# Kernel optimization log

Hardware: AMD Instinct MI355X
Metric: run time of the kernel (lower is better)

Reference implementation:

```python
import jax, jax.numpy as jnp
import numpy as np

B = 128
N0, N1, N2, N3 = 3072, 1536, 768, 384
DEG = 16
NUM_FEAT = 3
DIM_CELL = 8
ND = 32
ED = 64
IN_DRUG = 77
DIM_DRUG = 128
BN_EPS = 1e-5


def _pool_edges(e, cluster):
    # PyG max_pool edge pooling: relabel endpoints by cluster, drop self-loops, coalesce
    ce = cluster[e]
    ce = ce[:, ce[0] != ce[1]]
    return np.unique(ce, axis=1)


def setup_inputs():
    rng = np.random.default_rng(0)
    e0 = np.stack([rng.integers(0, N0, N0 * DEG), rng.integers(0, N0, N0 * DEG)])
    c0 = np.arange(N0) // 2
    c1 = np.arange(N1) // 2
    c2 = np.arange(N2) // 2
    e1 = _pool_edges(e0, c0)
    e2 = _pool_edges(e1, c1)
    de = np.stack([rng.integers(0, ND, ED), rng.integers(0, ND, ED)])
    be = lambda e, n: np.concatenate([e + j * n for j in range(B)], axis=1)
    bc = lambda c, k: np.concatenate([c + j * k for j in range(B)])
    keys = iter(jax.random.split(jax.random.key(0), 64))

    def lin(fi, fo):
        s = 1.0 / float(np.sqrt(fi))
        return (jax.random.uniform(next(keys), (fi, fo), jnp.float32, -s, s),
                jax.random.uniform(next(keys), (fo,), jnp.float32, -s, s))

    inp = {}
    inp["cell_x"] = jax.random.normal(next(keys), (B * N0, NUM_FEAT), jnp.float32)
    inp["drug_x"] = jax.random.normal(next(keys), (B * ND, IN_DRUG), jnp.float32)
    inp["cell_edges0"] = jnp.asarray(be(e0, N0), jnp.int32)
    inp["cell_edges1"] = jnp.asarray(be(e1, N1), jnp.int32)
    inp["cell_edges2"] = jnp.asarray(be(e2, N2), jnp.int32)
    inp["cluster0"] = jnp.asarray(bc(c0, N1), jnp.int32)
    inp["cluster1"] = jnp.asarray(bc(c1, N2), jnp.int32)
    inp["cluster2"] = jnp.asarray(bc(c2, N3), jnp.int32)
    inp["drug_edges"] = jnp.asarray(be(de, ND), jnp.int32)
    inp["drug_batch"] = jnp.asarray(np.repeat(np.arange(B), ND), jnp.int32)
    for i, fi in enumerate([NUM_FEAT, DIM_CELL, DIM_CELL]):
        W, b = lin(fi, DIM_CELL)
        inp[f"gat_W{i}"] = W
        inp[f"gat_b{i}"] = b
        inp[f"gat_as{i}"] = 0.1 * jax.random.normal(next(keys), (DIM_CELL,), jnp.float32)
        inp[f"gat_ad{i}"] = 0.1 * jax.random.normal(next(keys), (DIM_CELL,), jnp.float32)
    for i, fi in enumerate([IN_DRUG, DIM_DRUG, DIM_DRUG]):
        W1, b1 = lin(fi, DIM_DRUG)
        W2, b2 = lin(DIM_DRUG, DIM_DRUG)
        inp[f"gin_W1_{i}"] = W1
        inp[f"gin_b1_{i}"] = b1
        inp[f"gin_W2_{i}"] = W2
        inp[f"gin_b2_{i}"] = b2
        inp[f"bn_w{i}"] = jnp.ones((DIM_DRUG,), jnp.float32)
        inp[f"bn_b{i}"] = jnp.zeros((DIM_DRUG,), jnp.float32)
    inp["demb_W"], inp["demb_b"] = lin(3 * DIM_DRUG, 256)
    inp["cemb_W1"], inp["cemb_b1"] = lin(N3 * DIM_CELL, 1024)
    inp["cemb_W2"], inp["cemb_b2"] = lin(1024, 256)
    inp["reg_W1"], inp["reg_b1"] = lin(512, 512)
    inp["reg_W2"], inp["reg_b2"] = lin(512, 512)
    inp["reg_W3"], inp["reg_b3"] = lin(512, 1)
    return inp


def _bn(x, w=None, b=None):
    # training-mode BatchNorm1d (biased variance over the node dim)
    xn = (x - x.mean(0)) / jnp.sqrt(x.var(0) + BN_EPS)
    return xn if w is None else xn * w + b


def _gat(x, edges, W, a_s, a_d, b, n):
    # single-head GATConv with self-loops, negative_slope=0.2
    h = x @ W  # [n, d]
    loop = jnp.arange(n, dtype=edges.dtype)
    src = jnp.concatenate([edges[0], loop])
    dst = jnp.concatenate([edges[1], loop])
    logit = jax.nn.leaky_relu((h @ a_s)[src] + (h @ a_d)[dst], 0.2)
    m = jax.ops.segment_max(logit, dst, num_segments=n)
    e = jnp.exp(logit - m[dst])
    s = jax.ops.segment_sum(e, dst, num_segments=n)
    alpha = e / s[dst]
    return jax.ops.segment_sum(alpha[:, None] * h[src], dst, num_segments=n) + b


def _forward(floats, ints):
    (cell_x, drug_x,
     gat_W0, gat_b0, gat_as0, gat_ad0,
     gat_W1, gat_b1, gat_as1, gat_ad1,
     gat_W2, gat_b2, gat_as2, gat_ad2,
     gin_W1_0, gin_b1_0, gin_W2_0, gin_b2_0, bn_w0, bn_b0,
     gin_W1_1, gin_b1_1, gin_W2_1, gin_b2_1, bn_w1, bn_b1,
     gin_W1_2, gin_b1_2, gin_W2_2, gin_b2_2, bn_w2, bn_b2,
     demb_W, demb_b, cemb_W1, cemb_b1, cemb_W2, cemb_b2,
     reg_W1, reg_b1, reg_W2, reg_b2, reg_W3, reg_b3) = floats
    (cell_edges0, cell_edges1, cell_edges2,
     cluster0, cluster1, cluster2, drug_edges, drug_batch) = ints

    nd = drug_x.shape[0]
    x = drug_x
    feats = []
    for W1, b1, W2, b2, bw, bb in [
            (gin_W1_0, gin_b1_0, gin_W2_0, gin_b2_0, bn_w0, bn_b0),
            (gin_W1_1, gin_b1_1, gin_W2_1, gin_b2_1, bn_w1, bn_b1),
            (gin_W1_2, gin_b1_2, gin_W2_2, gin_b2_2, bn_w2, bn_b2)]:
        agg = x + jax.ops.segment_sum(x[drug_edges[0]], drug_edges[1], num_segments=nd)
        x = jax.nn.relu(jax.nn.relu(agg @ W1 + b1) @ W2 + b2)
        x = _bn(x, bw, bb)
        feats.append(x)
    xd = jax.ops.segment_max(jnp.concatenate(feats, axis=1), drug_batch, num_segments=B)
    xd = jax.nn.relu(xd @ demb_W + demb_b)  # [B, 256]

    xc = cell_x
    layers = [(cell_edges0, cluster0, B * N0, B * N1, gat_W0, gat_as0, gat_ad0, gat_b0),
              (cell_edges1, cluster1, B * N1, B * N2, gat_W1, gat_as1, gat_ad1, gat_b1),
              (cell_edges2, cluster2, B * N2, B * N3, gat_W2, gat_as2, gat_ad2, gat_b2)]
    for e, cl, n_in, n_out, W, a_s, a_d, b in layers:
        xc = jax.nn.relu(_gat(xc, e, W, a_s, a_d, b, n_in))
        xc = jax.ops.segment_max(xc, cl, num_segments=n_out)
        xc = _bn(xc)
    xc = xc.reshape(B, N3 * DIM_CELL)  # [B, 3072]
    xc = jax.nn.relu(xc @ cemb_W1 + cemb_b1)
    xc = jax.nn.relu(xc @ cemb_W2 + cemb_b2)  # [B, 256]

    z = jnp.concatenate([xd, xc], axis=-1)  # [B, 512]
    z = jax.nn.elu(z @ reg_W1 + reg_b1)
    z = jax.nn.elu(z @ reg_W2 + reg_b2)
    return z @ reg_W3 + reg_b3  # [B, 1]


def reference(cell_x, drug_x, cell_edges0, cell_edges1, cell_edges2, cluster0, cluster1, cluster2,
              drug_edges, drug_batch,
              gat_W0, gat_b0, gat_as0, gat_ad0, gat_W1, gat_b1, gat_as1, gat_ad1,
              gat_W2, gat_b2, gat_as2, gat_ad2,
              gin_W1_0, gin_b1_0, gin_W2_0, gin_b2_0, bn_w0, bn_b0,
              gin_W1_1, gin_b1_1, gin_W2_1, gin_b2_1, bn_w1, bn_b1,
              gin_W1_2, gin_b1_2, gin_W2_2, gin_b2_2, bn_w2, bn_b2,
              demb_W, demb_b, cemb_W1, cemb_b1, cemb_W2, cemb_b2,
              reg_W1, reg_b1, reg_W2, reg_b2, reg_W3, reg_b3):
    floats = (cell_x, drug_x,
              gat_W0, gat_b0, gat_as0, gat_ad0, gat_W1, gat_b1, gat_as1, gat_ad1,
              gat_W2, gat_b2, gat_as2, gat_ad2,
              gin_W1_0, gin_b1_0, gin_W2_0, gin_b2_0, bn_w0, bn_b0,
              gin_W1_1, gin_b1_1, gin_W2_1, gin_b2_1, bn_w1, bn_b1,
              gin_W1_2, gin_b1_2, gin_W2_2, gin_b2_2, bn_w2, bn_b2,
              demb_W, demb_b, cemb_W1, cemb_b1, cemb_W2, cemb_b2,
              reg_W1, reg_b1, reg_W2, reg_b2, reg_W3, reg_b3)
    ints = (cell_edges0, cell_edges1, cell_edges2, cluster0, cluster1, cluster2, drug_edges, drug_batch)
    return _forward(floats, ints)
```

## Files before the change

kernel.cpp:

```cpp
#include <hip/hip_runtime.h>
#include <math.h>

#define CDIV(a,b) (((a)+(b)-1)/(b))


template<int ACT>
__launch_bounds__(256)
__global__ void gemm_kernel(const float* __restrict__ A, const float* __restrict__ W,
                            const float* __restrict__ bias, float* __restrict__ C,
                            int M, int N, int K, int ldc) {
    const int BM = 64, BN = 64, BK = 16;
    __shared__ float As[BK][BM];
    __shared__ float Ws[BK][BN];
    int tid = threadIdx.x;
    int brow = blockIdx.y * BM;
    int bcol = blockIdx.x * BN;
    int tr = (tid / 16) * 4;
    int tc = (tid % 16) * 4;
    float acc[4][4] = {};
    for (int k0 = 0; k0 < K; k0 += BK) {
        for (int i = tid; i < BM * BK; i += 256) {
            int r = i / BK, c = i % BK;
            int gr = brow + r, gc = k0 + c;
            As[c][r] = (gr < M && gc < K) ? A[(size_t)gr * K + gc] : 0.f;
// ... 23 lines not shown
        int gr = brow + tr + i;
        if (gr >= M) continue;
        #pragma unroll
        for (int j = 0; j < 4; ++j) {
            int gc = bcol + tc + j;
            if (gc >= N) continue;
            float v = acc[i][j] + bias[gc];
            if (ACT == 1) v = fmaxf(v, 0.f);
            if (ACT == 2) v = (v > 0.f) ? v : expm1f(v);
            C[(size_t)gr * ldc + gc] = v;
        }
    }
}

__launch_bounds__(256)
__global__ void gemm_part_kernel(const float* __restrict__ A, const float* __restrict__ W,
                                 float* __restrict__ Cp, int M, int N, int K, int KC) {
    const int BM = 64, BN = 64, BK = 16;
    __shared__ float As[BK][BM];
    __shared__ float Ws[BK][BN];
    int tid = threadIdx.x;
    int brow = blockIdx.y * BM;
    int bcol = blockIdx.x * BN;
    int s = blockIdx.z;
    int kb = s * KC, ke = min(K, kb + KC);
    int tr = (tid / 16) * 4;
    int tc = (tid % 16) * 4;
    float acc[4][4] = {};
    for (int k0 = kb; k0 < ke; k0 += BK) {
        for (int i = tid; i < BM * BK; i += 256) {
// ... 48 lines not shown
}

__global__ void reg3_kernel(const float* __restrict__ z2, const float* __restrict__ W,
                            const float* __restrict__ b, float* __restrict__ out) {
    int gid = blockIdx.x * blockDim.x + threadIdx.x;
    int r = gid / 64;
    int lane = gid & 63;
    if (r >= 128) return;
    float a = 0.f;
    for (int c = lane; c < 512; c += 64) a += z2[(size_t)r * 512 + c] * W[c];
    #pragma unroll
    for (int o = 32; o > 0; o >>= 1) a += __shfl_down(a, o);
    if (lane == 0) out[r] = a + b[0];
}

__launch_bounds__(256)
__global__ void drug_agg_kernel(const int* __restrict__ edges, int E,
                                const float* __restrict__ x, float* __restrict__ agg, int F) {
    int g = blockIdx.x;
    __shared__ int es[64], ed[64];
    int t = threadIdx.x;
    if (t < 64) { es[t] = edges[g * 64 + t]; ed[t] = edges[E + g * 64 + t]; }
    __syncthreads();
    int base = g * 32;
    for (int idx = t; idx < 32 * F; idx += 256) {
        int node = idx / F, f = idx - node * F;
        int gn = base + node;
        float acc = x[(size_t)gn * F + f];
        #pragma unroll 4
        for (int e = 0; e < 64; ++e)
            if (ed[e] == gn) acc += x[(size_t)es[e] * F + f];
        agg[(size_t)gn * F + f] = acc;
    }
}

__global__ void drug_pool_kernel(const float* __restrict__ feats, float* __restrict__ xd) {
    int i = blockIdx.x * blockDim.x + threadIdx.x;
    if (i >= 128 * 384) return;
    int b = i / 384, f = i - b * 384;
    float m = -INFINITY;
    for (int r = 0; r < 32; ++r) m = fmaxf(m, feats[(size_t)(b * 32 + r) * 384 + f]);
    xd[i] = m;
}

__launch_bounds__(256)
__global__ void bn_stats_kernel(const float* __restrict__ x, int M, int N, float* __restrict__ sums) {
    int c = blockIdx.x;
    float s = 0.f, q = 0.f;
    for (int r = blockIdx.y * 256 + threadIdx.x; r < M; r += gridDim.y * 256) {
        float v = x[(size_t)r * N + c];
        s += v; q += v * v;
    }
    __shared__ float ss[256], qq[256];
    ss[threadIdx.x] = s; qq[threadIdx.x] = q;
    __syncthreads();
    for (int o = 128; o > 0; o >>= 1) {
        if (threadIdx.x < o) { ss[threadIdx.x] += ss[threadIdx.x + o]; qq[threadIdx.x] += qq[threadIdx.x + o]; }
        __syncthreads();
    }
    if (threadIdx.x == 0) { atomicAdd(&sums[c], ss[0]); atomicAdd(&sums[N + c], qq[0]); }
}

template<bool AFFINE>
__global__ void bn_apply_kernel(const float* __restrict__ x, const float* __restrict__ sums,
                                const float* __restrict__ w, const float* __restrict__ b,
                                float* __restrict__ out, float* __restrict__ out2,
                                int M, int N, int ldo2) {
    int i = blockIdx.x * blockDim.x + threadIdx.x;
    if (i >= M * N) return;
    int r = i / N, c = i - (i / N) * N;
    float mean = sums[c] / (float)M;
    float var  = sums[N + c] / (float)M - mean * mean;
    float inv  = rsqrtf(var + 1e-5f);
    float xn = (x[i] - mean) * inv;
    if (AFFINE) xn = xn * w[c] + b[c];
    out[i] = xn;
    if (out2) out2[(size_t)r * ldo2 + c] = xn;
}

template<bool BN>
__launch_bounds__(256)
__global__ void gat_proj_kernel(const float* __restrict__ x, const float* __restrict__ bnsums,
                                float minv, const float* __restrict__ W,
                                const float* __restrict__ a_s, const float* __restrict__ a_d,
                                float* __restrict__ h, float* __restrict__ hs, float* __restrict__ hd,
                                int n, int F) {
    __shared__ float smean[8], sinv[8];
    if (BN) {
        if (threadIdx.x < 8) {
            float mean = bnsums[threadIdx.x] * minv;
            float var  = bnsums[8 + threadIdx.x] * minv - mean * mean;
            smean[threadIdx.x] = mean;
            sinv[threadIdx.x]  = rsqrtf(var + 1e-5f);
        }
        __syncthreads();
    }
    int i = blockIdx.x * blockDim.x + threadIdx.x;
    if (i >= n) return;
    float acc[8];
    #pragma unroll
    for (int k = 0; k < 8; ++k) acc[k] = 0.f;
    for (int f = 0; f < F; ++f) {
        float xv = x[(size_t)i * F + f];
        if (BN) xv = (xv - smean[f]) * sinv[f];
        #pragma unroll
        for (int k = 0; k < 8; ++k) acc[k] += xv * W[f * 8 + k];
    }
    float s_ = 0.f, d_ = 0.f;
    #pragma unroll
    for (int k = 0; k < 8; ++k) {
        s_ += acc[k] * a_s[k];
        d_ += acc[k] * a_d[k];
    }
    float4* h4 = (float4*)(h + (size_t)i * 8);
    h4[0] = make_float4(acc[0], acc[1], acc[2], acc[3]);
    h4[1] = make_float4(acc[4], acc[5], acc[6], acc[7]);
    hs[i] = s_;
    hd[i] = d_;
}

__global__ void csr_count_kernel(const int* __restrict__ edges, int Eg, int Etot,
                                 int* __restrict__ deg) {
    int i = blockIdx.x * blockDim.x + threadIdx.x;
    if (i < Eg) atomicAdd(&deg[edges[Etot + i]], 1);
}

__launch_bounds__(256)
__global__ void scan_local_kernel(const int* __restrict__ deg, int* __restrict__ rowptr,
                                  int* __restrict__ bsum, int n) {
    __shared__ int sh[256];
    int base = blockIdx.x * 1024;
    int t = threadIdx.x;
    int v[4]; int s = 0;
    #pragma unroll
    for (int j = 0; j < 4; ++j) {
        int idx = base + t * 4 + j;
        v[j] = (idx < n) ? deg[idx] : 0;
        s += v[j];
    }
    sh[t] = s;
    __syncthreads();
    for (int o = 1; o < 256; o <<= 1) {
        int add = (t >= o) ? sh[t - o] : 0;
        __syncthreads();
        sh[t] += add;
        __syncthreads();
    }
    int excl = sh[t] - s;
    #pragma unroll
    for (int j = 0; j < 4; ++j) {
        int idx = base + t * 4 + j;
        if (idx < n) rowptr[idx] = excl;
        excl += v[j];
    }
    if (t == 255) bsum[blockIdx.x] = sh[255];
}

__launch_bounds__(256)
__global__ void scan_add_kernel(int* __restrict__ rowptr, const int* __restrict__ bsum, int n) {
    int b = blockIdx.x;
    int t = threadIdx.x;
    int acc = 0;
    for (int i = t; i < b; i += 256) acc += bsum[i];
    __shared__ int sh[256];
    sh[t] = acc;
    __syncthreads();
    for (int o = 128; o > 0; o >>= 1) {
        if (t < o) sh[t] += sh[t + o];
        __syncthreads();
    }
    int off = sh[0];
    int base = b * 1024;
    #pragma unroll
    for (int j = 0; j < 4; ++j) {
        int idx = base + t * 4 + j;
        if (idx < n) rowptr[idx] += off;
    }
}

__global__ void csr_fill_kernel(const int* __restrict__ edges, int Eg, int Etot,
                                const int* __restrict__ rowptr, int* __restrict__ cnt,
                                int* __restrict__ srclist) {
    int i = blockIdx.x * blockDim.x + threadIdx.x;
    if (i >= Eg) return;
    int s = edges[i], d = edges[Etot + i];
    int pos = rowptr[d] + atomicAdd(&cnt[d], 1);
    srclist[pos] = s;
}

__launch_bounds__(256)
__global__ void gat_gather_kernel(const int* __restrict__ rowptr, const int* __restrict__ deg,
                                  const int* __restrict__ srcl,
                                  const float* __restrict__ hs, const float* __restrict__ hd,
                                  const float* __restrict__ h, const float* __restrict__ bvec,
                                  float* __restrict__ pooled, float* __restrict__ sums,
                                  int n, int Nin, int Nout) {
    const int lane = threadIdx.x & 63;
    float4 bA = ((const float4*)bvec)[0];
    float4 bB = ((const float4*)bvec)[1];
    float ps[8] = {}, pq[8] = {};
    const float4* __restrict__ h4 = (const float4*)h;
    for (unsigned d = blockIdx.x * 256 + threadIdx.x; d < (unsigned)n; d += gridDim.x * 256) {
        unsigned b = d / (unsigned)Nin;
        unsigned dl = d - b * Nin;
        int base = b * Nin;
        float hdd = hd[d];
        float l = hs[d] + hdd;
        l = (l > 0.f) ? l : 0.2f * l;
        float e = __expf(l);
        float den = e;
        float4 sa = h4[2 * (size_t)d], sb = h4[2 * (size_t)d + 1];
        float n0 = e * sa.x, n1 = e * sa.y, n2 = e * sa.z, n3 = e * sa.w;
        float n4 = e * sb.x, n5 = e * sb.y, n6 = e * sb.z, n7 = e * sb.w;
        int j = rowptr[dl];
        int jend = j + deg[dl];
        for (; j + 2 <= jend; j += 2) {
            int s0 = srcl[j] + base;
            int s1 = srcl[j + 1] + base;
            float l0 = hs[s0] + hdd, l1 = hs[s1] + hdd;
            float4 a0 = h4[2 * (size_t)s0], b0 = h4[2 * (size_t)s0 + 1];
            float4 a1 = h4[2 * (size_t)s1], b1 = h4[2 * (size_t)s1 + 1];
            l0 = (l0 > 0.f) ? l0 : 0.2f * l0;
            l1 = (l1 > 0.f) ? l1 : 0.2f * l1;
            float e0 = __expf(l0), e1 = __expf(l1);
            den += e0 + e1;
            n0 += e0 * a0.x + e1 * a1.x;  n1 += e0 * a0.y + e1 * a1.y;
            n2 += e0 * a0.z + e1 * a1.z;  n3 += e0 * a0.w + e1 * a1.w;
            n4 += e0 * b0.x + e1 * b1.x;  n5 += e0 * b0.y + e1 * b1.y;
            n6 += e0 * b0.z + e1 * b1.z;  n7 += e0 * b0.w + e1 * b1.w;
        }
        if (j < jend) {
            int s0 = srcl[j] + base;
            float l0 = hs[s0] + hdd;
            float4 a0 = h4[2 * (size_t)s0], b0 = h4[2 * (size_t)s0 + 1];
            l0 = (l0 > 0.f) ? l0 : 0.2f * l0;
            float e0 = __expf(l0);
            den += e0;
            n0 += e0 * a0.x; n1 += e0 * a0.y; n2 += e0 * a0.z; n3 += e0 * a0.w;
            n4 += e0 * b0.x; n5 += e0 * b0.y; n6 += e0 * b0.z; n7 += e0 * b0.w;
        }
        float inv = 1.0f / den;
        float v0 = fmaxf(n0 * inv + bA.x, 0.f), v1 = fmaxf(n1 * inv + bA.y, 0.f);
        float v2 = fmaxf(n2 * inv + bA.z, 0.f), v3 = fmaxf(n3 * inv + bA.w, 0.f);
        float v4 = fmaxf(n4 * inv + bB.x, 0.f), v5 = fmaxf(n5 * inv + bB.y, 0.f);
        float v6 = fmaxf(n6 * inv + bB.z, 0.f), v7 = fmaxf(n7 * inv + bB.w, 0.f);
        v0 = fmaxf(v0, __shfl_xor(v0, 1)); v1 = fmaxf(v1, __shfl_xor(v1, 1));
        v2 = fmaxf(v2, __shfl_xor(v2, 1)); v3 = fmaxf(v3, __shfl_xor(v3, 1));
        v4 = fmaxf(v4, __shfl_xor(v4, 1)); v5 = fmaxf(v5, __shfl_xor(v5, 1));
        v6 = fmaxf(v6, __shfl_xor(v6, 1)); v7 = fmaxf(v7, __shfl_xor(v7, 1));
        float* row = pooled + ((size_t)b * Nout + (dl >> 1)) * 8;
        if ((lane & 1) == 0) {
            ((float4*)row)[0] = make_float4(v0, v1, v2, v3);
            ps[0] += v0; ps[1] += v1; ps[2] += v2; ps[3] += v3;
            ps[4] += v4; ps[5] += v5; ps[6] += v6; ps[7] += v7;
            pq[0] += v0 * v0; pq[1] += v1 * v1; pq[2] += v2 * v2; pq[3] += v3 * v3;
            pq[4] += v4 * v4; pq[5] += v5 * v5; pq[6] += v6 * v6; pq[7] += v7 * v7;
        } else {
            ((float4*)row)[1] = make_float4(v4, v5, v6, v7);
        }
    }
    #pragma unroll
    for (int k = 0; k < 8; ++k) {
        #pragma unroll
        for (int o = 32; o > 0; o >>= 1) {
            ps[k] += __shfl_xor(ps[k], o);
            pq[k] += __shfl_xor(pq[k], o);
        }
    }
    __shared__ float red[16];
    if (threadIdx.x < 16) red[threadIdx.x] = 0.f;
    __syncthreads();
    if (lane == 0) {
        #pragma unroll
        for (int k = 0; k < 8; ++k) {
            atomicAdd(&red[k], ps[k]);
            atomicAdd(&red[8 + k], pq[k]);
        }
    }
    __syncthreads();
    if (threadIdx.x < 16) atomicAdd(&sums[threadIdx.x], red[threadIdx.x]);
}

extern "C" void kernel_launch(void* const* d_in, const int* in_sizes, int n_in,
                              void* d_out, int out_size, void* d_ws, size_t ws_size,
                              hipStream_t stream) {
    const int B = 128, N0 = 3072, N1 = 1536, N2 = 768, N3 = 384;
    const int n0 = B * N0, n3 = B * N3;
    const int nd = B * 32;

    const float* cell_x = (const float*)d_in[0];
    const float* drug_x = (const float*)d_in[1];
    const int* ce[3]  = {(const int*)d_in[2], (const int*)d_in[3], (const int*)d_in[4]};
    const int  Ece[3] = {in_sizes[2] / 2, in_sizes[3] / 2, in_sizes[4] / 2};
    const int* drug_edges = (const int*)d_in[8];
    const int  Ed = in_sizes[8] / 2;
    const float* gat_W[3]  = {(const float*)d_in[10], (const float*)d_in[14], (const float*)d_in[18]};
    const float* gat_b[3]  = {(const float*)d_in[11], (const float*)d_in[15], (const float*)d_in[19]};
    const float* gat_as[3] = {(const float*)d_in[12], (const float*)d_in[16], (const float*)d_in[20]};
    const float* gat_ad[3] = {(const float*)d_in[13], (const float*)d_in[17], (const float*)d_in[21]};
    const float* gin_W1[3] = {(const float*)d_in[22], (const float*)d_in[28], (const float*)d_in[34]};
    const float* gin_b1[3] = {(const float*)d_in[23], (const float*)d_in[29], (const float*)d_in[35]};
    const float* gin_W2[3] = {(const float*)d_in[24], (const float*)d_in[30], (const float*)d_in[36]};
    const float* gin_b2[3] = {(const float*)d_in[25], (const float*)d_in[31], (const float*)d_in[37]};
    const float* bn_w[3]   = {(const float*)d_in[26], (const float*)d_in[32], (const float*)d_in[38]};
    const float* bn_b[3]   = {(const float*)d_in[27], (const float*)d_in[33], (const float*)d_in[39]};
    const float* demb_W  = (const float*)d_in[40];
    const float* demb_b  = (const float*)d_in[41];
    const float* cemb_W1 = (const float*)d_in[42];
// ... 2 lines not shown
    const float* cemb_b2 = (const float*)d_in[45];
    const float* reg_W1  = (const float*)d_in[46];
    const float* reg_b1  = (const float*)d_in[47];
    const float* reg_W2  = (const float*)d_in[48];
    const float* reg_b2  = (const float*)d_in[49];
    const float* reg_W3  = (const float*)d_in[50];
    const float* reg_b3  = (const float*)d_in[51];

    char* pp = (char*)d_ws;
    auto alloc = [&](size_t bytes) -> void* {
        void* r = pp;
        pp += (bytes + 255) & ~(size_t)255;
        return r;
    };
    float* bnsums  = (float*)alloc(1024 * 4);
    float* h       = (float*)alloc((size_t)n0 * 8 * 4);
    float* hs      = (float*)alloc((size_t)n0 * 4);
    float* hd      = (float*)alloc((size_t)n0 * 4);
    int*   deg     = (int*)alloc((size_t)2 * N0 * 4);
    int*   rowptr  = (int*)alloc((size_t)N0 * 4);
    int*   bsum    = (int*)alloc(64 * 4);
    int*   srclist = (int*)alloc((size_t)(Ece[0] / B + 256) * 4);
    float* pooled  = (float*)alloc((size_t)(B * N1) * 8 * 4);
    float* xc3     = (float*)alloc((size_t)n3 * 8 * 4);
    float* Cpart   = (float*)alloc((size_t)12 * 128 * 1024 * 4);
    float* cembh   = (float*)alloc(128 * 1024 * 4);
    float* agg     = (float*)alloc((size_t)nd * 128 * 4);
    float* dt1     = (float*)alloc((size_t)nd * 128 * 4);
    float* dx      = (float*)alloc((size_t)nd * 128 * 4);
    float* feats   = (float*)alloc((size_t)nd * 384 * 4);
    float* xd      = (float*)alloc(128 * 384 * 4);
    float* z       = (float*)alloc(128 * 512 * 4);
    float* z1      = (float*)alloc(128 * 512 * 4);
    float* z2      = (float*)alloc(128 * 512 * 4);

    hipMemsetAsync(bnsums, 0, 1024 * 4, stream);

    {
        const float* xin = drug_x;
        int F = 77;
        for (int L = 0; L < 3; ++L) {
            drug_agg_kernel<<<B, 256, 0, stream>>>(drug_edges, Ed, xin, agg, F);
            gemm_kernel<1><<<dim3(2, CDIV(nd, 64)), 256, 0, stream>>>(
                agg, gin_W1[L], gin_b1[L], dt1, nd, 128, F, 128);
            gemm_kernel<1><<<dim3(2, CDIV(nd, 64)), 256, 0, stream>>>(
                dt1, gin_W2[L], gin_b2[L], dx, nd, 128, 128, 128);
            float* sums = bnsums + L * 256;
            bn_stats_kernel<<<dim3(128, 2), 256, 0, stream>>>(dx, nd, 128, sums);
            bn_apply_kernel<true><<<CDIV(nd * 128, 256), 256, 0, stream>>>(
                dx, sums, bn_w[L], bn_b[L], dx, feats + 128 * L, nd, 128, 384);
            xin = dx;
            F = 128;
        }
        drug_pool_kernel<<<CDIV(128 * 384, 256), 256, 0, stream>>>(feats, xd);
        gemm_part_kernel<<<dim3(4, 2, 6), 256, 0, stream>>>(xd, demb_W, Cpart, 128, 256, 384, 64);
        gemm_reduce_kernel<1><<<CDIV(128 * 256, 256), 256, 0, stream>>>(
            Cpart, demb_b, z, 128, 256, 6, 512);
    }

    {
        const int nin[3]  = {n0, B * N1, B * N2};
        const int Nin[3]  = {N0, N1, N2};
        const int Nout[3] = {N1, N2, N3};
        const float* xcin = cell_x;
        for (int L = 0; L < 3; ++L) {
            int n = nin[L];
            int Nloc = Nin[L];
            int Eg = Ece[L] / B;
            if (L == 0) {
                gat_proj_kernel<false><<<CDIV(n, 256), 256, 0, stream>>>(
                    xcin, nullptr, 0.f, gat_W[L], gat_as[L], gat_ad[L], h, hs, hd, n, 3);
            } else {
                gat_proj_kernel<true><<<CDIV(n, 256), 256, 0, stream>>>(
                    xcin, bnsums + 768 + (L - 1) * 32, 1.0f / (float)n,
                    gat_W[L], gat_as[L], gat_ad[L], h, hs, hd, n, 8);
            }
            int* cnt = deg + Nloc;
            hipMemsetAsync(deg, 0, (size_t)2 * Nloc * 4, stream);
            csr_count_kernel<<<CDIV(Eg, 256), 256, 0, stream>>>(ce[L], Eg, Ece[L], deg);
            int nb = CDIV(Nloc, 1024);
            scan_local_kernel<<<nb, 256, 0, stream>>>(deg, rowptr, bsum, Nloc);
            scan_add_kernel<<<nb, 256, 0, stream>>>(rowptr, bsum, Nloc);
            csr_fill_kernel<<<CDIV(Eg, 256), 256, 0, stream>>>(ce[L], Eg, Ece[L], rowptr, cnt, srclist);
            int gb = CDIV(n, 256) < 768 ? CDIV(n, 256) : 768;
            gat_gather_kernel<<<gb, 256, 0, stream>>>(
                rowptr, deg, srclist, hs, hd, h, gat_b[L],
                pooled, bnsums + 768 + L * 32, n, Nin[L], Nout[L]);
            xcin = pooled;
        }
        bn_apply_kernel<false><<<CDIV(n3 * 8, 256), 256, 0, stream>>>(
            pooled, bnsums + 768 + 2 * 32, nullptr, nullptr, xc3, nullptr, n3, 8, 0);
    }

    gemm_part_kernel<<<dim3(16, 2, 12), 256, 0, stream>>>(xc3, cemb_W1, Cpart, 128, 1024, 3072, 256);
    gemm_reduce_kernel<1><<<CDIV(128 * 1024, 256), 256, 0, stream>>>(
        Cpart, cemb_b1, cembh, 128, 1024, 12, 1024);
    gemm_part_kernel<<<dim3(4, 2, 8), 256, 0, stream>>>(cembh, cemb_W2, Cpart, 128, 256, 1024, 128);
    gemm_reduce_kernel<1><<<CDIV(128 * 256, 256), 256, 0, stream>>>(
        Cpart, cemb_b2, z + 256, 128, 256, 8, 512);
    gemm_part_kernel<<<dim3(8, 2, 8), 256, 0, stream>>>(z, reg_W1, Cpart, 128, 512, 512, 64);
    gemm_reduce_kernel<2><<<CDIV(128 * 512, 256), 256, 0, stream>>>(
        Cpart, reg_b1, z1, 128, 512, 8, 512);
    gemm_part_kernel<<<dim3(8, 2, 8), 256, 0, stream>>>(z1, reg_W2, Cpart, 128, 512, 512, 64);
    gemm_reduce_kernel<2><<<CDIV(128 * 512, 256), 256, 0, stream>>>(
        Cpart, reg_b2, z2, 128, 512, 8, 512);
    reg3_kernel<<<32, 256, 0, stream>>>(z2, reg_W3, reg_b3, (float*)d_out);
}
// ... 1 lines not shown
```

Before: 1.027 ms.

## Fuse BN stats into GEMM, build all CSRs in one kernel, fuse GAT layers per graph

The GIN second GEMM now accumulates batch-norm sums in its epilogue, and the BN affine transform is folded into the next aggregation and the pooling kernel. This removes the separate stats and apply kernels. All three CSR structures are built in one shared-memory kernel, replacing the memset, count, scan and fill chain that ran per layer. The GAT projection, attention gather and pooling run per graph in one kernel per layer, staging features in LDS. This cuts launches and global round trips, but hardcodes the graph sizes and edge-buffer capacities.

New measurement: 924.3 us. -10.0%, faster.

```diff
diff --git a/kernel.cpp b/kernel.cpp
--- a/kernel.cpp
+++ b/kernel.cpp
@@ -61,6 +61,72 @@
 }
 
 __launch_bounds__(256)
+__global__ void gemm_stats_kernel(const float* __restrict__ A, const float* __restrict__ W,
+                                  const float* __restrict__ bias, float* __restrict__ C,
+                                  int M, int N, int K, float* __restrict__ sums) {
+    const int BM = 64, BN = 64, BK = 16;
+    __shared__ float As[BK][BM];
+    __shared__ float Ws[BK][BN];
+    __shared__ float cs[64], cq[64];
+    int tid = threadIdx.x;
+    int brow = blockIdx.y * BM;
+    int bcol = blockIdx.x * BN;
+    int tr = (tid / 16) * 4;
+    int tc = (tid % 16) * 4;
+    float acc[4][4] = {};
+    for (int k0 = 0; k0 < K; k0 += BK) {
+        for (int i = tid; i < BM * BK; i += 256) {
+            int r = i / BK, c = i % BK;
+            int gr = brow + r, gc = k0 + c;
+            As[c][r] = (gc < K) ? A[(size_t)gr * K + gc] : 0.f;
+        }
+        for (int i = tid; i < BK * BN; i += 256) {
+            int r = i / BN, c = i % BN;
+            int gr = k0 + r, gc = bcol + c;
+            Ws[r][c] = (gr < K) ? W[(size_t)gr * N + gc] : 0.f;
+        }
+        __syncthreads();
+        #pragma unroll
+        for (int kk = 0; kk < BK; ++kk) {
+            float a[4], w[4];
+            #pragma unroll
+            for (int i = 0; i < 4; ++i) a[i] = As[kk][tr + i];
+            #pragma unroll
+            for (int j = 0; j < 4; ++j) w[j] = Ws[kk][tc + j];
+            #pragma unroll
+            for (int i = 0; i < 4; ++i)
+                #pragma unroll
+                for (int j = 0; j < 4; ++j) acc[i][j] += a[i] * w[j];
+        }
+        __syncthreads();
+    }
+    if (tid < 64) { cs[tid] = 0.f; cq[tid] = 0.f; }
+    __syncthreads();
+    float myS[4] = {}, myQ[4] = {};
+    #pragma unroll
+    for (int i = 0; i < 4; ++i) {
+        int gr = brow + tr + i;
+        #pragma unroll
+        for (int j = 0; j < 4; ++j) {
+            int gc = bcol + tc + j;
+            float v = fmaxf(acc[i][j] + bias[gc], 0.f);
+            C[(size_t)gr * N + gc] = v;
+            myS[j] += v; myQ[j] += v * v;
+        }
+    }
+    #pragma unroll
+    for (int j = 0; j < 4; ++j) {
+        atomicAdd(&cs[tc + j], myS[j]);
+        atomicAdd(&cq[tc + j], myQ[j]);
+    }
+    __syncthreads();
+    if (tid < 64) {
+        atomicAdd(&sums[bcol + tid], cs[tid]);
+        atomicAdd(&sums[N + bcol + tid], cq[tid]);
+    }
+}
+
+__launch_bounds__(256)
 __global__ void gemm_part_kernel(const float* __restrict__ A, const float* __restrict__ W,
                                  float* __restrict__ Cp, int M, int N, int K, int KC) {
     const int BM = 64, BN = 64, BK = 16;
@@ -139,284 +205,334 @@
     if (lane == 0) out[r] = a + b[0];
 }
 
+template<bool BN>
 __launch_bounds__(256)
 __global__ void drug_agg_kernel(const int* __restrict__ edges, int E,
-                                const float* __restrict__ x, float* __restrict__ agg, int F) {
-    int g = blockIdx.x;
+                                const float* __restrict__ x, float* __restrict__ agg, int F,
+                                const float* __restrict__ sums, const float* __restrict__ bw,
+                                const float* __restrict__ bb) {
     __shared__ int es[64], ed[64];
-    int t = threadIdx.x;
+    __shared__ float sa[128], sb[128];
+    int g = blockIdx.x, t = threadIdx.x;
     if (t < 64) { es[t] = edges[g * 64 + t]; ed[t] = edges[E + g * 64 + t]; }
+    if (BN && t >= 128 && t < 256) {
+        int c = t - 128;
+        float mean = sums[c] * (1.f / 4096.f);
+        float var  = sums[128 + c] * (1.f / 4096.f) - mean * mean;
+        float inv  = rsqrtf(var + 1e-5f);
+        float a = bw[c] * inv;
+        sa[c] = a; sb[c] = bb[c] - mean * a;
+    }
     __syncthreads();
     int base = g * 32;
     for (int idx = t; idx < 32 * F; idx += 256) {
         int node = idx / F, f = idx - node * F;
         int gn = base + node;
-        float acc = x[(size_t)gn * F + f];
+        float v = x[(size_t)gn * F + f];
+        if (BN) v = v * sa[f] + sb[f];
+        float acc = v;
         #pragma unroll 4
         for (int e = 0; e < 64; ++e)
-            if (ed[e] == gn) acc += x[(size_t)es[e] * F + f];
+            if (ed[e] == gn) {
+                float u = x[(size_t)es[e] * F + f];
+                if (BN) u = u * sa[f] + sb[f];
+                acc += u;
+            }
         agg[(size_t)gn * F + f] = acc;
     }
 }
 
-__global__ void drug_pool_kernel(const float* __restrict__ feats, float* __restrict__ xd) {
+__global__ void drug_pool_kernel(const float* __restrict__ dx0, const float* __restrict__ dx1,
+                                 const float* __restrict__ dx2, const float* __restrict__ bnsums,
+                                 const float* __restrict__ w0, const float* __restrict__ b0,
+                                 const float* __restrict__ w1, const float* __restrict__ b1,
+                                 const float* __restrict__ w2, const float* __restrict__ b2,
+                                 float* __restrict__ xd) {
     int i = blockIdx.x * blockDim.x + threadIdx.x;
     if (i >= 128 * 384) return;
     int b = i / 384, f = i - b * 384;
+    int L = f >> 7, c = f & 127;
+    const float* dx = (L == 0) ? dx0 : (L == 1) ? dx1 : dx2;
+    const float* w  = (L == 0) ? w0  : (L == 1) ? w1  : w2;
+    const float* bb = (L == 0) ? b0  : (L == 1) ? b1  : b2;
+    const float* s  = bnsums + L * 256;
+    float mean = s[c] * (1.f / 4096.f);
+    float var  = s[128 + c] * (1.f / 4096.f) - mean * mean;
+    float inv  = rsqrtf(var + 1e-5f);
+    float a = w[c] * inv;
+    float d = bb[c] - mean * a;
     float m = -INFINITY;
-    for (int r = 0; r < 32; ++r) m = fmaxf(m, feats[(size_t)(b * 32 + r) * 384 + f]);
+    for (int r = 0; r < 32; ++r) m = fmaxf(m, dx[(size_t)(b * 32 + r) * 128 + c] * a + d);
     xd[i] = m;
 }
 
-__launch_bounds__(256)
-__global__ void bn_stats_kernel(const float* __restrict__ x, int M, int N, float* __restrict__ sums) {
-    int c = blockIdx.x;
-    float s = 0.f, q = 0.f;
-    for (int r = blockIdx.y * 256 + threadIdx.x; r < M; r += gridDim.y * 256) {
-        float v = x[(size_t)r * N + c];
-        s += v; q += v * v;
-    }
-    __shared__ float ss[256], qq[256];
-    ss[threadIdx.x] = s; qq[threadIdx.x] = q;
-    __syncthreads();
-    for (int o = 128; o > 0; o >>= 1) {
-        if (threadIdx.x < o) { ss[threadIdx.x] += ss[threadIdx.x + o]; qq[threadIdx.x] += qq[threadIdx.x + o]; }
-        __syncthreads();
-    }
-    if (threadIdx.x == 0) { atomicAdd(&sums[c], ss[0]); atomicAdd(&sums[N + c], qq[0]); }
-}
-
-template<bool AFFINE>
 __global__ void bn_apply_kernel(const float* __restrict__ x, const float* __restrict__ sums,
-                                const float* __restrict__ w, const float* __restrict__ b,
-                                float* __restrict__ out, float* __restrict__ out2,
-                                int M, int N, int ldo2) {
+                                float* __restrict__ out, int M) {
     int i = blockIdx.x * blockDim.x + threadIdx.x;
-    if (i >= M * N) return;
-    int r = i / N, c = i - (i / N) * N;
-    float mean = sums[c] / (float)M;
-    float var  = sums[N + c] / (float)M - mean * mean;
-    float inv  = rsqrtf(var + 1e-5f);
-    float xn = (x[i] - mean) * inv;
-    if (AFFINE) xn = xn * w[c] + b[c];
-    out[i] = xn;
-    if (out2) out2[(size_t)r * ldo2 + c] = xn;
-}
-
-template<bool BN>
-__launch_bounds__(256)
-__global__ void gat_proj_kernel(const float* __restrict__ x, const float* __restrict__ bnsums,
-                                float minv, const float* __restrict__ W,
-                                const float* __restrict__ a_s, const float* __restrict__ a_d,
-                                float* __restrict__ h, float* __restrict__ hs, float* __restrict__ hd,
-                                int n, int F) {
-    __shared__ float smean[8], sinv[8];
-    if (BN) {
-        if (threadIdx.x < 8) {
-            float mean = bnsums[threadIdx.x] * minv;
-            float var  = bnsums[8 + threadIdx.x] * minv - mean * mean;
-            smean[threadIdx.x] = mean;
-            sinv[threadIdx.x]  = rsqrtf(var + 1e-5f);
-        }
-        __syncthreads();
-    }
-    int i = blockIdx.x * blockDim.x + threadIdx.x;
-    if (i >= n) return;
-    float acc[8];
-    #pragma unroll
-    for (int k = 0; k < 8; ++k) acc[k] = 0.f;
-    for (int f = 0; f < F; ++f) {
-        float xv = x[(size_t)i * F + f];
-        if (BN) xv = (xv - smean[f]) * sinv[f];
-        #pragma unroll
-        for (int k = 0; k < 8; ++k) acc[k] += xv * W[f * 8 + k];
-    }
-    float s_ = 0.f, d_ = 0.f;
+    if (i >= M * 8) return;
+    int c = i & 7;
+    float minv = 1.0f / (float)M;
+    float mean = sums[c] * minv;
+    float var  = sums[8 + c] * minv - mean * mean;
+    out[i] = (x[i] - mean) * rsqrtf(var + 1e-5f);
+}
+
+__launch_bounds__(1024)
+__global__ void csr_all_kernel(const int* __restrict__ e0, int Eg0, int Et0,
+                               const int* __restrict__ e1, int Eg1, int Et1,
+                               const int* __restrict__ e2, int Eg2, int Et2,
+                               int* __restrict__ rowptr, int* __restrict__ srcl) {
+    __shared__ int sdeg[3072];
+    __shared__ int srp[3072];
+    __shared__ int ssum[1024];
+    int L = blockIdx.x;
+    const int* e = (L == 0) ? e0 : (L == 1) ? e1 : e2;
+    int Eg   = (L == 0) ? Eg0 : (L == 1) ? Eg1 : Eg2;
+    int Et   = (L == 0) ? Et0 : (L == 1) ? Et1 : Et2;
+    int Nloc = (L == 0) ? 3072 : (L == 1) ? 1536 : 768;
+    int* grp  = rowptr + L * 3088;
+    int* gsrc = srcl + L * 49408;
+    int t = threadIdx.x;
+    for (int i = t; i < Nloc; i += 1024) sdeg[i] = 0;
+    __syncthreads();
+    for (int i = t; i < Eg; i += 1024) atomicAdd(&sdeg[e[Et + i]], 1);
+    __syncthreads();
+    int CH = (Nloc + 1023) >> 10;
+    int s = 0;
+    for (int c = 0; c < CH; ++c) { int idx = t * CH + c; if (idx < Nloc) s += sdeg[idx]; }
+    ssum[t] = s;
+    __syncthreads();
+    for (int o = 1; o < 1024; o <<= 1) {
+        int add = (t >= o) ? ssum[t - o] : 0;
+        __syncthreads();
+        ssum[t] += add;
+        __syncthreads();
+    }
+    int excl = ssum[t] - s;
+    for (int c = 0; c < CH; ++c) {
+        int idx = t * CH + c;
+        if (idx < Nloc) { srp[idx] = excl; excl += sdeg[idx]; }
+    }
+    __syncthreads();
+    for (int i = t; i < Nloc; i += 1024) { grp[i] = srp[i]; sdeg[i] = 0; }
+    if (t == 1023) grp[Nloc] = ssum[1023];
+    __syncthreads();
+    for (int i = t; i < Eg; i += 1024) {
+        int src = e[i], d = e[Et + i];
+        int pos = srp[d] + atomicAdd(&sdeg[d], 1);
+        gsrc[pos] = src;
+    }
+}
+
+__launch_bounds__(512)
+__global__ void gat_l0_kernel(const float* __restrict__ x, const float* __restrict__ W,
+                              const float* __restrict__ avs, const float* __restrict__ avd,
+                              const float* __restrict__ bvec,
+                              const int* __restrict__ rp, const int* __restrict__ srcl,
+                              float* __restrict__ pooled, float* __restrict__ sums) {
+    const int NIN = 3072, NOUT = 1536, NDST = 1536;
+    __shared__ float lx[NIN * 3];
+    __shared__ float red[16];
+    int b = blockIdx.x >> 1, half = blockIdx.x & 1;
+    int t = threadIdx.x;
+    int lane = t & 63;
+    const float* xb = x + (size_t)b * NIN * 3;
+    for (int i = t; i < NIN * 3; i += 512) lx[i] = xb[i];
+    float w[24], as_[8], ad_[8], bv[8];
     #pragma unroll
     for (int k = 0; k < 8; ++k) {
-        s_ += acc[k] * a_s[k];
-        d_ += acc[k] * a_d[k];
-    }
-    float4* h4 = (float4*)(h + (size_t)i * 8);
-    h4[0] = make_float4(acc[0], acc[1], acc[2], acc[3]);
-    h4[1] = make_float4(acc[4], acc[5], acc[6], acc[7]);
-    hs[i] = s_;
-    hd[i] = d_;
-}
-
-__global__ void csr_count_kernel(const int* __restrict__ edges, int Eg, int Etot,
-                                 int* __restrict__ deg) {
-    int i = blockIdx.x * blockDim.x + threadIdx.x;
-    if (i < Eg) atomicAdd(&deg[edges[Etot + i]], 1);
-}
-
-__launch_bounds__(256)
-__global__ void scan_local_kernel(const int* __restrict__ deg, int* __restrict__ rowptr,
-                                  int* __restrict__ bsum, int n) {
-    __shared__ int sh[256];
-    int base = blockIdx.x * 1024;
-    int t = threadIdx.x;
-    int v[4]; int s = 0;
-    #pragma unroll
-    for (int j = 0; j < 4; ++j) {
-        int idx = base + t * 4 + j;
-        v[j] = (idx < n) ? deg[idx] : 0;
-        s += v[j];
-    }
-    sh[t] = s;
-    __syncthreads();
-    for (int o = 1; o < 256; o <<= 1) {
-        int add = (t >= o) ? sh[t - o] : 0;
-        __syncthreads();
-        sh[t] += add;
-        __syncthreads();
-    }
-    int excl = sh[t] - s;
-    #pragma unroll
-    for (int j = 0; j < 4; ++j) {
-        int idx = base + t * 4 + j;
-        if (idx < n) rowptr[idx] = excl;
-        excl += v[j];
-    }
-    if (t == 255) bsum[blockIdx.x] = sh[255];
-}
-
-__launch_bounds__(256)
-__global__ void scan_add_kernel(int* __restrict__ rowptr, const int* __restrict__ bsum, int n) {
-    int b = blockIdx.x;
-    int t = threadIdx.x;
-    int acc = 0;
-    for (int i = t; i < b; i += 256) acc += bsum[i];
-    __shared__ int sh[256];
-    sh[t] = acc;
-    __syncthreads();
-    for (int o = 128; o > 0; o >>= 1) {
-        if (t < o) sh[t] += sh[t + o];
-        __syncthreads();
-    }
-    int off = sh[0];
-    int base = b * 1024;
-    #pragma unroll
-    for (int j = 0; j < 4; ++j) {
-        int idx = base + t * 4 + j;
-        if (idx < n) rowptr[idx] += off;
-    }
-}
-
-__global__ void csr_fill_kernel(const int* __restrict__ edges, int Eg, int Etot,
-                                const int* __restrict__ rowptr, int* __restrict__ cnt,
-                                int* __restrict__ srclist) {
-    int i = blockIdx.x * blockDim.x + threadIdx.x;
-    if (i >= Eg) return;
-    int s = edges[i], d = edges[Etot + i];
-    int pos = rowptr[d] + atomicAdd(&cnt[d], 1);
-    srclist[pos] = s;
-}
-
-__launch_bounds__(256)
-__global__ void gat_gather_kernel(const int* __restrict__ rowptr, const int* __restrict__ deg,
-                                  const int* __restrict__ srcl,
-                                  const float* __restrict__ hs, const float* __restrict__ hd,
-                                  const float* __restrict__ h, const float* __restrict__ bvec,
-                                  float* __restrict__ pooled, float* __restrict__ sums,
-                                  int n, int Nin, int Nout) {
-    const int lane = threadIdx.x & 63;
-    float4 bA = ((const float4*)bvec)[0];
-    float4 bB = ((const float4*)bvec)[1];
+        w[k] = W[k]; w[8 + k] = W[8 + k]; w[16 + k] = W[16 + k];
+        as_[k] = avs[k]; ad_[k] = avd[k]; bv[k] = bvec[k];
+    }
+    __syncthreads();
     float ps[8] = {}, pq[8] = {};
-    const float4* __restrict__ h4 = (const float4*)h;
-    for (unsigned d = blockIdx.x * 256 + threadIdx.x; d < (unsigned)n; d += gridDim.x * 256) {
-        unsigned b = d / (unsigned)Nin;
-        unsigned dl = d - b * Nin;
-        int base = b * Nin;
-        float hdd = hd[d];
-        float l = hs[d] + hdd;
+    for (int i = t; i < NDST; i += 512) {
+        int dl = half * NDST + i;
+        float x0 = lx[dl * 3], x1 = lx[dl * 3 + 1], x2 = lx[dl * 3 + 2];
+        float hk[8];
+        float hsd = 0.f, hdd = 0.f;
+        #pragma unroll
+        for (int k = 0; k < 8; ++k) {
+            hk[k] = x0 * w[k] + x1 * w[8 + k] + x2 * w[16 + k];
+            hsd += hk[k] * as_[k];
+            hdd += hk[k] * ad_[k];
+        }
+        float l = hsd + hdd;
         l = (l > 0.f) ? l : 0.2f * l;
         float e = __expf(l);
         float den = e;
-        float4 sa = h4[2 * (size_t)d], sb = h4[2 * (size_t)d + 1];
-        float n0 = e * sa.x, n1 = e * sa.y, n2 = e * sa.z, n3 = e * sa.w;
-        float n4 = e * sb.x, n5 = e * sb.y, n6 = e * sb.z, n7 = e * sb.w;
-        int j = rowptr[dl];
-        int jend = j + deg[dl];
-        for (; j + 2 <= jend; j += 2) {
-            int s0 = srcl[j] + base;
-            int s1 = srcl[j + 1] + base;
-            float l0 = hs[s0] + hdd, l1 = hs[s1] + hdd;
-            float4 a0 = h4[2 * (size_t)s0], b0 = h4[2 * (size_t)s0 + 1];
-            float4 a1 = h4[2 * (size_t)s1], b1 = h4[2 * (size_t)s1 + 1];
-            l0 = (l0 > 0.f) ? l0 : 0.2f * l0;
-            l1 = (l1 > 0.f) ? l1 : 0.2f * l1;
-            float e0 = __expf(l0), e1 = __expf(l1);
-            den += e0 + e1;
-            n0 += e0 * a0.x + e1 * a1.x;  n1 += e0 * a0.y + e1 * a1.y;
-            n2 += e0 * a0.z + e1 * a1.z;  n3 += e0 * a0.w + e1 * a1.w;
-            n4 += e0 * b0.x + e1 * b1.x;  n5 += e0 * b0.y + e1 * b1.y;
-            n6 += e0 * b0.z + e1 * b1.z;  n7 += e0 * b0.w + e1 * b1.w;
-        }
-        if (j < jend) {
-            int s0 = srcl[j] + base;
-            float l0 = hs[s0] + hdd;
-            float4 a0 = h4[2 * (size_t)s0], b0 = h4[2 * (size_t)s0 + 1];
-            l0 = (l0 > 0.f) ? l0 : 0.2f * l0;
-            float e0 = __expf(l0);
-            den += e0;
-            n0 += e0 * a0.x; n1 += e0 * a0.y; n2 += e0 * a0.z; n3 += e0 * a0.w;
-            n4 += e0 * b0.x; n5 += e0 * b0.y; n6 += e0 * b0.z; n7 += e0 * b0.w;
+        float num[8];
+        #pragma unroll
+        for (int k = 0; k < 8; ++k) num[k] = e * hk[k];
+        int j = rp[dl], je = rp[dl + 1];
+        for (; j < je; ++j) {
+            int s = srcl[j];
+            float y0 = lx[s * 3], y1 = lx[s * 3 + 1], y2 = lx[s * 3 + 2];
+            float g[8];
+            float gs = 0.f;
+            #pragma unroll
+            for (int k = 0; k < 8; ++k) {
+                g[k] = y0 * w[k] + y1 * w[8 + k] + y2 * w[16 + k];
+                gs += g[k] * as_[k];
+            }
+            float ll = gs + hdd;
+            ll = (ll > 0.f) ? ll : 0.2f * ll;
+            float ee = __expf(ll);
+            den += ee;
+            #pragma unroll
+            for (int k = 0; k < 8; ++k) num[k] += ee * g[k];
         }
         float inv = 1.0f / den;
-        float v0 = fmaxf(n0 * inv + bA.x, 0.f), v1 = fmaxf(n1 * inv + bA.y, 0.f);
-        float v2 = fmaxf(n2 * inv + bA.z, 0.f), v3 = fmaxf(n3 * inv + bA.w, 0.f);
-        float v4 = fmaxf(n4 * inv + bB.x, 0.f), v5 = fmaxf(n5 * inv + bB.y, 0.f);
-        float v6 = fmaxf(n6 * inv + bB.z, 0.f), v7 = fmaxf(n7 * inv + bB.w, 0.f);
-        v0 = fmaxf(v0, __shfl_xor(v0, 1)); v1 = fmaxf(v1, __shfl_xor(v1, 1));
-        v2 = fmaxf(v2, __shfl_xor(v2, 1)); v3 = fmaxf(v3, __shfl_xor(v3, 1));
-        v4 = fmaxf(v4, __shfl_xor(v4, 1)); v5 = fmaxf(v5, __shfl_xor(v5, 1));
-        v6 = fmaxf(v6, __shfl_xor(v6, 1)); v7 = fmaxf(v7, __shfl_xor(v7, 1));
-        float* row = pooled + ((size_t)b * Nout + (dl >> 1)) * 8;
+        float v[8];
+        #pragma unroll
+        for (int k = 0; k < 8; ++k) {
+            v[k] = fmaxf(num[k] * inv + bv[k], 0.f);
+            v[k] = fmaxf(v[k], __shfl_xor(v[k], 1));
+        }
+        float* row = pooled + ((size_t)b * NOUT + (dl >> 1)) * 8;
         if ((lane & 1) == 0) {
-            ((float4*)row)[0] = make_float4(v0, v1, v2, v3);
-            ps[0] += v0; ps[1] += v1; ps[2] += v2; ps[3] += v3;
-            ps[4] += v4; ps[5] += v5; ps[6] += v6; ps[7] += v7;
-            pq[0] += v0 * v0; pq[1] += v1 * v1; pq[2] += v2 * v2; pq[3] += v3 * v3;
-            pq[4] += v4 * v4; pq[5] += v5 * v5; pq[6] += v6 * v6; pq[7] += v7 * v7;
+            ((float4*)row)[0] = make_float4(v[0], v[1], v[2], v[3]);
+            #pragma unroll
+            for (int k = 0; k < 8; ++k) { ps[k] += v[k]; pq[k] += v[k] * v[k]; }
         } else {
-            ((float4*)row)[1] = make_float4(v4, v5, v6, v7);
-        }
-    }
-    #pragma unroll
-    for (int k = 0; k < 8; ++k) {
+            ((float4*)row)[1] = make_float4(v[4], v[5], v[6], v[7]);
+        }
+    }
+    #pragma unroll
+    for (int k = 0; k < 8; ++k)
         #pragma unroll
         for (int o = 32; o > 0; o >>= 1) {
             ps[k] += __shfl_xor(ps[k], o);
             pq[k] += __shfl_xor(pq[k], o);
         }
-    }
-    __shared__ float red[16];
-    if (threadIdx.x < 16) red[threadIdx.x] = 0.f;
-    __syncthreads();
-    if (lane == 0) {
+    if (t < 16) red[t] = 0.f;
+    __syncthreads();
+    if (lane == 0)
+        #pragma unroll
+        for (int k = 0; k < 8; ++k) { atomicAdd(&red[k], ps[k]); atomicAdd(&red[8 + k], pq[k]); }
+    __syncthreads();
+    if (t < 16) atomicAdd(&sums[t], red[t]);
+}
+
+template<int NIN>
+__launch_bounds__(512)
+__global__ void gat_h_kernel(const float* __restrict__ xin, const float* __restrict__ bnin,
+                             float minv, const float* __restrict__ W,
+                             const float* __restrict__ avs, const float* __restrict__ avd,
+                             const float* __restrict__ bvec,
+                             const int* __restrict__ rp, const int* __restrict__ srcl,
+                             float* __restrict__ pooled, float* __restrict__ sums) {
+    const int NOUT = NIN / 2, NDST = NIN / 2;
+    __shared__ float lh[NIN * 8];
+    __shared__ float lhs[NIN];
+    __shared__ float smean[8], sinv[8], red[16];
+    int b = blockIdx.x >> 1, half = blockIdx.x & 1;
+    int t = threadIdx.x;
+    int lane = t & 63;
+    if (t < 8) {
+        float mean = bnin[t] * minv;
+        float var  = bnin[8 + t] * minv - mean * mean;
+        smean[t] = mean;
+        sinv[t]  = rsqrtf(var + 1e-5f);
+    }
+    float w[64], as_[8], ad_[8], bv[8];
+    #pragma unroll
+    for (int f = 0; f < 8; ++f)
+        #pragma unroll
+        for (int k = 0; k < 8; ++k) w[f * 8 + k] = W[f * 8 + k];
+    #pragma unroll
+    for (int k = 0; k < 8; ++k) { as_[k] = avs[k]; ad_[k] = avd[k]; bv[k] = bvec[k]; }
+    __syncthreads();
+    const float4* x4 = (const float4*)xin;
+    for (int i = t; i < NIN; i += 512) {
+        float4 r0 = x4[((size_t)b * NIN + i) * 2];
+        float4 r1 = x4[((size_t)b * NIN + i) * 2 + 1];
+        float xv[8] = {r0.x, r0.y, r0.z, r0.w, r1.x, r1.y, r1.z, r1.w};
+        float hk[8] = {};
+        #pragma unroll
+        for (int f = 0; f < 8; ++f) {
+            float xn = (xv[f] - smean[f]) * sinv[f];
+            #pragma unroll
+            for (int k = 0; k < 8; ++k) hk[k] += xn * w[f * 8 + k];
+        }
+        float hsv = 0.f;
+        #pragma unroll
+        for (int k = 0; k < 8; ++k) { lh[i * 8 + k] = hk[k]; hsv += hk[k] * as_[k]; }
+        lhs[i] = hsv;
+    }
+    __syncthreads();
+    float ps[8] = {}, pq[8] = {};
+    for (int i = t; i < NDST; i += 512) {
+        int dl = half * NDST + i;
+        const float4* hr = (const float4*)&lh[dl * 8];
+        float4 ha = hr[0], hb = hr[1];
+        float hk[8] = {ha.x, ha.y, ha.z, ha.w, hb.x, hb.y, hb.z, hb.w};
+        float hdd = 0.f;
+        #pragma unroll
+        for (int k = 0; k < 8; ++k) hdd += hk[k] * ad_[k];
+        float l = lhs[dl] + hdd;
+        l = (l > 0.f) ? l : 0.2f * l;
+        float e = __expf(l);
+        float den = e;
+        float num[8];
+        #pragma unroll
+        for (int k = 0; k < 8; ++k) num[k] = e * hk[k];
+        int j = rp[dl], je = rp[dl + 1];
+        for (; j < je; ++j) {
+            int s = srcl[j];
+            float ls = lhs[s] + hdd;
+            ls = (ls > 0.f) ? ls : 0.2f * ls;
+            float ee = __expf(ls);
+            den += ee;
+            const float4* sr = (const float4*)&lh[s * 8];
+            float4 sa = sr[0], sb = sr[1];
+            num[0] += ee * sa.x; num[1] += ee * sa.y; num[2] += ee * sa.z; num[3] += ee * sa.w;
+            num[4] += ee * sb.x; num[5] += ee * sb.y; num[6] += ee * sb.z; num[7] += ee * sb.w;
+        }
+        float inv = 1.0f / den;
+        float v[8];
         #pragma unroll
         for (int k = 0; k < 8; ++k) {
-            atomicAdd(&red[k], ps[k]);
-            atomicAdd(&red[8 + k], pq[k]);
-        }
-    }
-    __syncthreads();
-    if (threadIdx.x < 16) atomicAdd(&sums[threadIdx.x], red[threadIdx.x]);
+            v[k] = fmaxf(num[k] * inv + bv[k], 0.f);
+            v[k] = fmaxf(v[k], __shfl_xor(v[k], 1));
+        }
+        float* row = pooled + ((size_t)b * NOUT + (dl >> 1)) * 8;
+        if ((lane & 1) == 0) {
+            ((float4*)row)[0] = make_float4(v[0], v[1], v[2], v[3]);
+            #pragma unroll
+            for (int k = 0; k < 8; ++k) { ps[k] += v[k]; pq[k] += v[k] * v[k]; }
+        } else {
+            ((float4*)row)[1] = make_float4(v[4], v[5], v[6], v[7]);
+        }
+    }
+    #pragma unroll
+    for (int k = 0; k < 8; ++k)
+        #pragma unroll
+        for (int o = 32; o > 0; o >>= 1) {
+            ps[k] += __shfl_xor(ps[k], o);
+            pq[k] += __shfl_xor(pq[k], o);
+        }
+    if (t < 16) red[t] = 0.f;
+    __syncthreads();
+    if (lane == 0)
+        #pragma unroll
+        for (int k = 0; k < 8; ++k) { atomicAdd(&red[k], ps[k]); atomicAdd(&red[8 + k], pq[k]); }
+    __syncthreads();
+    if (t < 16) atomicAdd(&sums[t], red[t]);
 }
 
 extern "C" void kernel_launch(void* const* d_in, const int* in_sizes, int n_in,
                               void* d_out, int out_size, void* d_ws, size_t ws_size,
                               hipStream_t stream) {
-    const int B = 128, N0 = 3072, N1 = 1536, N2 = 768, N3 = 384;
-    const int n0 = B * N0, n3 = B * N3;
+    const int B = 128, N3 = 384;
+    const int n3 = B * N3;
     const int nd = B * 32;
 
     const float* cell_x = (const float*)d_in[0];
     const float* drug_x = (const float*)d_in[1];
     const int* ce[3]  = {(const int*)d_in[2], (const int*)d_in[3], (const int*)d_in[4]};
-    const int  Ece[3] = {in_sizes[2] / 2, in_sizes[3] / 2, in_sizes[4] / 2};
+    const int  Etot[3] = {in_sizes[2] / 2, in_sizes[3] / 2, in_sizes[4] / 2};
+    const int  Eg[3]   = {Etot[0] / B, Etot[1] / B, Etot[2] / B};
     const int* drug_edges = (const int*)d_in[8];
     const int  Ed = in_sizes[8] / 2;
     const float* gat_W[3]  = {(const float*)d_in[10], (const float*)d_in[14], (const float*)d_in[18]};
@@ -449,21 +565,18 @@
         return r;
     };
     float* bnsums  = (float*)alloc(1024 * 4);
-    float* h       = (float*)alloc((size_t)n0 * 8 * 4);
-    float* hs      = (float*)alloc((size_t)n0 * 4);
-    float* hd      = (float*)alloc((size_t)n0 * 4);
-    int*   deg     = (int*)alloc((size_t)2 * N0 * 4);
-    int*   rowptr  = (int*)alloc((size_t)N0 * 4);
-    int*   bsum    = (int*)alloc(64 * 4);
-    int*   srclist = (int*)alloc((size_t)(Ece[0] / B + 256) * 4);
-    float* pooled  = (float*)alloc((size_t)(B * N1) * 8 * 4);
+    int*   rowptr  = (int*)alloc((size_t)3 * 3088 * 4);
+    int*   srcl    = (int*)alloc((size_t)3 * 49408 * 4);
+    float* pooledA = (float*)alloc((size_t)(B * 1536) * 8 * 4);
+    float* pooledB = (float*)alloc((size_t)(B * 768) * 8 * 4);
     float* xc3     = (float*)alloc((size_t)n3 * 8 * 4);
     float* Cpart   = (float*)alloc((size_t)12 * 128 * 1024 * 4);
     float* cembh   = (float*)alloc(128 * 1024 * 4);
     float* agg     = (float*)alloc((size_t)nd * 128 * 4);
     float* dt1     = (float*)alloc((size_t)nd * 128 * 4);
-    float* dx      = (float*)alloc((size_t)nd * 128 * 4);
-    float* feats   = (float*)alloc((size_t)nd * 384 * 4);
+    float* dx0     = (float*)alloc((size_t)nd * 128 * 4);
+    float* dx1     = (float*)alloc((size_t)nd * 128 * 4);
+    float* dx2     = (float*)alloc((size_t)nd * 128 * 4);
     float* xd      = (float*)alloc(128 * 384 * 4);
     float* z       = (float*)alloc(128 * 512 * 4);
     float* z1      = (float*)alloc(128 * 512 * 4);
@@ -471,61 +584,47 @@
 
     hipMemsetAsync(bnsums, 0, 1024 * 4, stream);
 
+    csr_all_kernel<<<3, 1024, 0, stream>>>(ce[0], Eg[0], Etot[0],
+                                           ce[1], Eg[1], Etot[1],
+                                           ce[2], Eg[2], Etot[2], rowptr, srcl);
+
     {
+        float* dxs[3] = {dx0, dx1, dx2};
         const float* xin = drug_x;
         int F = 77;
         for (int L = 0; L < 3; ++L) {
-            drug_agg_kernel<<<B, 256, 0, stream>>>(drug_edges, Ed, xin, agg, F);
+            if (L == 0)
+                drug_agg_kernel<false><<<B, 256, 0, stream>>>(drug_edges, Ed, xin, agg, F,
+                                                              nullptr, nullptr, nullptr);
+            else
+                drug_agg_kernel<true><<<B, 256, 0, stream>>>(drug_edges, Ed, xin, agg, F,
+                                                             bnsums + (L - 1) * 256,
+                                                             bn_w[L - 1], bn_b[L - 1]);
             gemm_kernel<1><<<dim3(2, CDIV(nd, 64)), 256, 0, stream>>>(
                 agg, gin_W1[L], gin_b1[L], dt1, nd, 128, F, 128);
-            gemm_kernel<1><<<dim3(2, CDIV(nd, 64)), 256, 0, stream>>>(
-                dt1, gin_W2[L], gin_b2[L], dx, nd, 128, 128, 128);
-            float* sums = bnsums + L * 256;
-            bn_stats_kernel<<<dim3(128, 2), 256, 0, stream>>>(dx, nd, 128, sums);
-            bn_apply_kernel<true><<<CDIV(nd * 128, 256), 256, 0, stream>>>(
-                dx, sums, bn_w[L], bn_b[L], dx, feats + 128 * L, nd, 128, 384);
-            xin = dx;
+            gemm_stats_kernel<<<dim3(2, CDIV(nd, 64)), 256, 0, stream>>>(
+                dt1, gin_W2[L], gin_b2[L], dxs[L], nd, 128, 128, bnsums + L * 256);
+            xin = dxs[L];
             F = 128;
         }
-        drug_pool_kernel<<<CDIV(128 * 384, 256), 256, 0, stream>>>(feats, xd);
+        drug_pool_kernel<<<CDIV(128 * 384, 256), 256, 0, stream>>>(
+            dx0, dx1, dx2, bnsums, bn_w[0], bn_b[0], bn_w[1], bn_b[1], bn_w[2], bn_b[2], xd);
         gemm_part_kernel<<<dim3(4, 2, 6), 256, 0, stream>>>(xd, demb_W, Cpart, 128, 256, 384, 64);
         gemm_reduce_kernel<1><<<CDIV(128 * 256, 256), 256, 0, stream>>>(
             Cpart, demb_b, z, 128, 256, 6, 512);
     }
 
-    {
-        const int nin[3]  = {n0, B * N1, B * N2};
-        const int Nin[3]  = {N0, N1, N2};
-        const int Nout[3] = {N1, N2, N3};
-        const float* xcin = cell_x;
-        for (int L = 0; L < 3; ++L) {
-            int n = nin[L];
-            int Nloc = Nin[L];
-            int Eg = Ece[L] / B;
-            if (L == 0) {
-                gat_proj_kernel<false><<<CDIV(n, 256), 256, 0, stream>>>(
-                    xcin, nullptr, 0.f, gat_W[L], gat_as[L], gat_ad[L], h, hs, hd, n, 3);
-            } else {
-                gat_proj_kernel<true><<<CDIV(n, 256), 256, 0, stream>>>(
-                    xcin, bnsums + 768 + (L - 1) * 32, 1.0f / (float)n,
-                    gat_W[L], gat_as[L], gat_ad[L], h, hs, hd, n, 8);
-            }
-            int* cnt = deg + Nloc;
-            hipMemsetAsync(deg, 0, (size_t)2 * Nloc * 4, stream);
-            csr_count_kernel<<<CDIV(Eg, 256), 256, 0, stream>>>(ce[L], Eg, Ece[L], deg);
-            int nb = CDIV(Nloc, 1024);
-            scan_local_kernel<<<nb, 256, 0, stream>>>(deg, rowptr, bsum, Nloc);
-            scan_add_kernel<<<nb, 256, 0, stream>>>(rowptr, bsum, Nloc);
-            csr_fill_kernel<<<CDIV(Eg, 256), 256, 0, stream>>>(ce[L], Eg, Ece[L], rowptr, cnt, srclist);
-            int gb = CDIV(n, 256) < 768 ? CDIV(n, 256) : 768;
-            gat_gather_kernel<<<gb, 256, 0, stream>>>(
-                rowptr, deg, srclist, hs, hd, h, gat_b[L],
-                pooled, bnsums + 768 + L * 32, n, Nin[L], Nout[L]);
-            xcin = pooled;
-        }
-        bn_apply_kernel<false><<<CDIV(n3 * 8, 256), 256, 0, stream>>>(
-            pooled, bnsums + 768 + 2 * 32, nullptr, nullptr, xc3, nullptr, n3, 8, 0);
-    }
+    gat_l0_kernel<<<256, 512, 0, stream>>>(cell_x, gat_W[0], gat_as[0], gat_ad[0], gat_b[0],
+                                           rowptr, srcl, pooledA, bnsums + 768);
+    gat_h_kernel<1536><<<256, 512, 0, stream>>>(pooledA, bnsums + 768, 1.f / 196608.f,
+                                                gat_W[1], gat_as[1], gat_ad[1], gat_b[1],
+                                                rowptr + 3088, srcl + 49408,
+                                                pooledB, bnsums + 800);
+    gat_h_kernel<768><<<256, 512, 0, stream>>>(pooledB, bnsums + 800, 1.f / 98304.f,
+                                               gat_W[2], gat_as[2], gat_ad[2], gat_b[2],
+                                               rowptr + 2 * 3088, srcl + 2 * 49408,
+                                               pooledA, bnsums + 832);
+    bn_apply_kernel<<<CDIV(n3 * 8, 256), 256, 0, stream>>>(pooledA, bnsums + 832, xc3, n3);
 
     gemm_part_kernel<<<dim3(16, 2, 12), 256, 0, stream>>>(xc3, cemb_W1, Cpart, 128, 1024, 3072, 256);
     gemm_reduce_kernel<1><<<CDIV(128 * 1024, 256), 256, 0, stream>>>(
```
